# Optimization experiments

Measured on AMD Instinct MI355X. Metric: run time of the kernel, lower is better.

## Reference

```python
import jax, jax.numpy as jnp
import numpy as np
from jax import lax


def get_grid(h, w):
    # normalized [-1,1] grid, channel 0 = x, channel 1 = y, shape [1,h,w,2]
    gx, gy = jnp.meshgrid(jnp.linspace(-1.0, 1.0, w), jnp.linspace(-1.0, 1.0, h))
    return jnp.stack([gx, gy], axis=-1)[None].astype(jnp.float32)


def gaussian_kernel(k, sigma=1.0):
    c = jnp.arange(k, dtype=jnp.float32) - (k - 1) / 2.0
    g = jnp.exp(-(c ** 2) / (2.0 * sigma ** 2))
    k2 = jnp.outer(g, g)
    return k2 / k2.sum()


def resize_bilinear(x, H, W):
    # x: [B,C,h,w]; torch F.interpolate(mode='bilinear', align_corners=False)
    B, C, h, w = x.shape
    def coords(n_out, n_in):
        c = (jnp.arange(n_out, dtype=jnp.float32) + 0.5) * (n_in / n_out) - 0.5
        c = jnp.clip(c, 0.0, n_in - 1.0)
        lo = jnp.floor(c).astype(jnp.int32)
        hi = jnp.minimum(lo + 1, n_in - 1)
        return lo, hi, c - lo.astype(jnp.float32)
    y0, y1, wy = coords(H, h)
    x0, x1, wx = coords(W, w)
    r = x[:, :, y0, :] * (1.0 - wy)[None, None, :, None] + x[:, :, y1, :] * wy[None, None, :, None]
    return r[:, :, :, x0] * (1.0 - wx) + r[:, :, :, x1] * wx


def _forward(src_grid, kernel, src_grid_base, tgt_grid, niter):
    B = src_grid.shape[0]
    H, W = tgt_grid.shape[1], tgt_grid.shape[2]
    ks = kernel.shape[-1]
    HW = H * W
    # forward displacement, resampled to target resolution, in pixel units
    dsrc = (src_grid - src_grid_base).transpose(0, 3, 1, 2)        # [B,2,Hs,Ws]
    dsrc = resize_bilinear(dsrc, H, W)                              # [B,2,H,W]
    dx = dsrc[:, 0].reshape(B, HW) * (W / 2.0)
    dy = dsrc[:, 1].reshape(B, HW) * (H / 2.0)
    xg = (jnp.arange(HW) % W).astype(jnp.float32)
    yg = (jnp.arange(HW) // W).astype(jnp.float32)
    xi = jnp.round(xg[None] + dx).astype(jnp.int32)
    yi = jnp.round(yg[None] + dy).astype(jnp.int32)
    oob = (xi < 0) | (yi < 0) | (xi > W - 1) | (yi > H - 1)
    field = jnp.where(oob, -1, yi * W + xi) + 1   # index 0 = trash slot
    # sort + dedup: duplicates are redirected to the trash slot
    order = jnp.argsort(field, axis=1)            # stable
    sf = jnp.take_along_axis(field, order, axis=1)
    keep = jnp.concatenate([jnp.ones((B, 1), bool), sf[:, 1:] != sf[:, :-1]], axis=1)
    sf = sf * keep
    inv_order = jnp.argsort(order, axis=1)
    field = jnp.take_along_axis(sf, inv_order, axis=1)
    # scatter inverse displacement (unique indices except trash slot 0)
    z = jnp.zeros((B, 1), dtype=dx.dtype)
    dxp = jnp.concatenate([z, dx], axis=1)
    dyp = jnp.concatenate([z, dy], axis=1)
    fieldp = jnp.concatenate([jnp.zeros((B, 1), field.dtype), field], axis=1)
    bidx = jnp.arange(B)[:, None]
    inv_dx = jnp.zeros_like(dxp).at[bidx, fieldp].set(-dxp)[:, 1:].reshape(B, H, W)
    inv_dy = jnp.zeros_like(dyp).at[bidx, fieldp].set(-dyp)[:, 1:].reshape(B, H, W)
    mask = (jnp.zeros_like(dxp).at[bidx, fieldp].set(1.0)[:, 1:].reshape(B, H, W)) > 0.5
    # pad so hole-fill never reads outside
    p = niter + 1
    inv_dx = jnp.pad(inv_dx, ((0, 0), (p, p), (p, p)))
    inv_dy = jnp.pad(inv_dy, ((0, 0), (p, p), (p, p)))
    mask = jnp.pad(mask, ((0, 0), (p, p), (p, p)))
    pd = ks // 2
    k4 = kernel.reshape(1, 1, ks, ks)
    def conv(x):
        return lax.conv_general_dilated(x[:, None], k4, (1, 1), [(pd, pd), (pd, pd)])[:, 0]
    # hole-fill: dilate mask by 4-neighborhood, fill with gaussian-weighted avg
    for _ in range(niter):
        nb = (jnp.pad(mask, ((0, 0), (1, 0), (0, 0)))[:, :-1]
              | jnp.pad(mask, ((0, 0), (0, 1), (0, 0)))[:, 1:]
              | jnp.pad(mask, ((0, 0), (0, 0), (1, 0)))[:, :, :-1]
              | jnp.pad(mask, ((0, 0), (0, 0), (0, 1)))[:, :, 1:])
        new_mask = (~mask) & nb
        new_dx = conv(inv_dx)
        new_dy = conv(inv_dy)
        new_sum = conv(mask.astype(inv_dx.dtype))
        denom = jnp.where(new_mask, new_sum, 1.0)  # safe: new_sum>0 where new_mask
        inv_dx = jnp.where(new_mask, new_dx / denom, inv_dx)
        inv_dy = jnp.where(new_mask, new_dy / denom, inv_dy)
        mask = mask | new_mask
    # erode: drop pixels with any unmasked 4-neighbor (outside counts as masked)
    for _ in range(niter):
        full = (jnp.pad(mask, ((0, 0), (1, 0), (0, 0)), constant_values=True)[:, :-1]
                & jnp.pad(mask, ((0, 0), (0, 1), (0, 0)), constant_values=True)[:, 1:]
                & jnp.pad(mask, ((0, 0), (0, 0), (1, 0)), constant_values=True)[:, :, :-1]
                & jnp.pad(mask, ((0, 0), (0, 0), (0, 1)), constant_values=True)[:, :, 1:])
        mask = mask & full
    inv_dx = jnp.where(mask, inv_dx, 2.0 * W)
    inv_dy = jnp.where(mask, inv_dy, 2.0 * H)
    inv_dx = inv_dx[:, p:-p, p:-p]
    inv_dy = inv_dy[:, p:-p, p:-p]
    dtgt = jnp.stack([inv_dx * (2.0 / W), inv_dy * (2.0 / H)], axis=3)
    return tgt_grid + dtgt


def setup_inputs() -> dict:
    key = jax.random.key(0)
    B, Hs, Ws, H, W = 8, 256, 256, 512, 512
    base = get_grid(Hs, Ws)
    src_grid = base + 0.05 * jax.random.normal(key, (B, Hs, Ws, 2), jnp.float32)
    return {
        "src_grid": src_grid,
        "kernel": gaussian_kernel(3),
        "src_grid_base": base,
        "tgt_grid": get_grid(H, W),
        "niter": 5,
    }


def reference(src_grid, kernel, src_grid_base, tgt_grid, niter):
    return _forward(src_grid, kernel, src_grid_base, tgt_grid, niter)
```

## Files before the change

kernel.cpp:

```cpp
#include <hip/hip_runtime.h>
#include <hip/hip_fp16.h>

typedef unsigned long long u64;
typedef unsigned int u32;
typedef float float4a __attribute__((ext_vector_type(4), aligned(4)));

#define B_    8
#define HS_   256
#define WS_   256
#define H_    512
#define W_    512
#define HW_   (H_ * W_)
#define TO_Y  8
#define NTILE 64
#define WR    28
#define WCOLS 276
#define WSTR  277
#define NBAND 32
#define NBKT  64
#define INFW  0xFFFFFFFFu
#define CAPB  8192

__device__ __forceinline__ void bilin_disp(const float* __restrict__ src,
                                           const float* __restrict__ base,
                                           int b, int y, int x,
                                           float& dx, float& dy) {
#pragma clang fp contract(off)
    float cy = ((float)y + 0.5f) * 0.5f - 0.5f;
    cy = fminf(fmaxf(cy, 0.0f), 255.0f);
    int   y0 = (int)floorf(cy);
    int   y1 = min(y0 + 1, HS_ - 1);
    float wy = cy - (float)y0;

    float cx = ((float)x + 0.5f) * 0.5f - 0.5f;
    cx = fminf(fmaxf(cx, 0.0f), 255.0f);
    int   x0 = (int)floorf(cx);
    float wx = cx - (float)x0;

    float omy = 1.0f - wy;
    float wA, wB;
    int xs;
    if (x0 >= WS_ - 1) { xs = WS_ - 2; wA = 0.0f; wB = 1.0f; }
    else               { xs = x0;      wA = 1.0f - wx; wB = wx; }

    const float4a* S0 = (const float4a*)(src  + ((b * HS_ + y0) * WS_ + xs) * 2);
    const float4a* S1 = (const float4a*)(src  + ((b * HS_ + y1) * WS_ + xs) * 2);
    const float4a* B0 = (const float4a*)(base + (y0 * WS_ + xs) * 2);
    const float4a* B1 = (const float4a*)(base + (y1 * WS_ + xs) * 2);
    float4a s0 = *S0, s1 = *S1, b0 = *B0, b1 = *B1;

    float a00x = s0.x - b0.x, a00y = s0.y - b0.y;
    float a01x = s0.z - b0.z, a01y = s0.w - b0.w;
    float a10x = s1.x - b1.x, a10y = s1.y - b1.y;
    float a11x = s1.z - b1.z, a11y = s1.w - b1.w;

    float r0x = a00x * omy + a10x * wy;
    float r0y = a00y * omy + a10y * wy;
    float r1x = a01x * omy + a11x * wy;
    float r1y = a01y * omy + a11y * wy;
    dx = (r0x * wA + r1x * wB) * 256.0f;
    dy = (r0y * wA + r1y * wB) * 256.0f;
}

__device__ __forceinline__ u32 pack16(float x, float y) {
    __half hx = __float2half_rn(x), hy = __float2half_rn(y);
    return ((u32)__half_as_ushort(hy) << 16) | (u32)__half_as_ushort(hx);
}
__device__ __forceinline__ float2 unpack16(u32 p) {
    float2 f;
    f.x = __half2float(__ushort_as_half((unsigned short)(p & 0xFFFFu)));
    f.y = __half2float(__ushort_as_half((unsigned short)(p >> 16)));
    return f;
}

__device__ __forceinline__ u64 shfl_left(u64 v) {
    unsigned lo = __shfl_up((unsigned)v, 1);
    unsigned hi = __shfl_up((unsigned)(v >> 32), 1);
    u64 r = ((u64)hi << 32) | lo;
    return (threadIdx.x & 63) ? r : 0ull;
}
__device__ __forceinline__ u64 shfl_right(u64 v) {
    unsigned lo = __shfl_down((unsigned)v, 1);
    unsigned hi = __shfl_down((unsigned)(v >> 32), 1);
    u64 r = ((u64)hi << 32) | lo;
    return ((threadIdx.x & 63) == 63) ? 0ull : r;
}

__launch_bounds__(1024)
__global__ void pre_k(const float* __restrict__ src,
                      const float* __restrict__ base,
                      u32* __restrict__ pay,
                      u32* __restrict__ gcount,
                      u32* __restrict__ bucket) {
    __shared__ u32 cnt[NBKT];
    __shared__ u32 bbase[NBKT];

    int bid = blockIdx.x;
    int b   = bid & 7;
    int t   = bid >> 3;
    int j   = t * 1024 + threadIdx.x;
    int y   = j >> 9;
    int x   = j & (W_ - 1);

    if (threadIdx.x < NBKT) cnt[threadIdx.x] = 0;
    __syncthreads();

    float dx, dy;
    bilin_disp(src, base, b, y, x, dx, dy);
    pay[b * HW_ + j] = pack16(-dx, -dy);

    int xi = (int)rintf((float)x + dx);
    int yi = (int)rintf((float)y + dy);
    bool inb = (xi >= 0 && xi < W_ && yi >= 0 && yi < H_);
    int bk0 = 0, bk1 = -1;
    u32 r0 = 0, r1 = 0, e = 0;
    if (inb) {
        int band = yi >> 4;
        bk0 = band * 2 + (xi >> 8);
        r0 = atomicAdd(&cnt[bk0], 1u);
        if      (xi >= 246 && xi <= 255) bk1 = band * 2 + 1;
        else if (xi >= 256 && xi <= 265) bk1 = band * 2;
        if (bk1 >= 0) r1 = atomicAdd(&cnt[bk1], 1u);
        e = ((u32)(yi & 15) << 27) | ((u32)xi << 18) | (u32)j;
    }
    __syncthreads();
    if (threadIdx.x < NBKT) {
        u32 c = cnt[threadIdx.x];
        bbase[threadIdx.x] = c ? atomicAdd(&gcount[b * NBKT + threadIdx.x], c)
                               : 0u;
    }
    __syncthreads();
    if (inb) {
        u32 s0 = bbase[bk0] + r0;
        if (s0 < CAPB) bucket[(b * NBKT + bk0) * CAPB + s0] = e;
        if (bk1 >= 0) {
            u32 s1 = bbase[bk1] + r1;
            if (s1 < CAPB) bucket[(b * NBKT + bk1) * CAPB + s1] = e;
        }
    }
}

__launch_bounds__(512, 2)
__global__ void fused5_k(const u32* __restrict__ pay,
                         const u32* __restrict__ gcount,
                         const u32* __restrict__ bucket,
                         const float* __restrict__ kern,
                         const float* __restrict__ tgt,
                         float* __restrict__ out) {
    __shared__ u32 plane[WR * WSTR];

    int id   = blockIdx.x;
    int b    = id & 7;
    int rest = id >> 3;
    int tile = rest >> 1;
    int half = rest & 1;
    int X0   = half << 8;
    int Y0   = tile * TO_Y;
    int w0   = Y0 - 10;
    int wc0  = X0 - 10;
    int tid  = threadIdx.x;

    float kw[9];
#pragma unroll
    for (int q = 0; q < 9; q++) kw[q] = kern[q];

    for (int i = tid; i < WR * WSTR; i += 512) plane[i] = INFW;
    __syncthreads();

    {
        int qlo = max(0, w0 >> 4);
        int qhi = min(NBAND - 1, (w0 + WR - 1) >> 4);
        for (int q = qlo; q <= qhi; q++) {
            int bki = b * NBKT + q * 2 + half;
            u32 cntq = min(gcount[bki], (u32)CAPB);
            const u32* bk = bucket + bki * CAPB;
            int ybase = q * 16 - w0;
            for (u32 i = tid; i < cntq; i += 512) {
                u32 e  = bk[i];
                int wr = ybase + (int)((e >> 27) & 15u);
                if ((unsigned)wr < WR) {
                    int xc = (int)((e >> 18) & 511u) - wc0;
                    atomicMin(&plane[wr * WSTR + xc], e & 0x3FFFFu);
                }
            }
        }
    }
    __syncthreads();

    int wv   = tid >> 6;
    int lane = tid & 63;
    int col  = X0 + 32 * wv - 16 + lane;
    int cls  = col - wc0;
    bool inwin = ((unsigned)cls < WCOLS);
    bool colin = inwin && (col >= -6) && (col <= W_ + 5);

    u64 m = 0;
    if (colin) {
#pragma unroll 7
        for (int r = 0; r < WR; r++)
            m |= (u64)(plane[r * WSTR + cls] != INFW) << r;
    }
    __syncthreads();

    {
        const u32* pb = pay + b * HW_;
        for (int idx = tid; idx < WR * WCOLS; idx += 512) {
            int rr = idx / WCOLS;
            int cc = idx - rr * WCOLS;
            int off = rr * WSTR + cc;
            u32 k = plane[off];
            plane[off] = (k != INFW) ? pb[k] : 0u;
        }
    }
    __syncthreads();

    int rlo = max(0, -6 - w0);
    int rhi = min(WR - 1, (W_ + 5) - w0);
    u64 validm = colin ? ((((u64)1 << (rhi - rlo + 1)) - 1) << rlo) : 0ull;

    const u64 VROWS = (((u64)1 << (WR - 12)) - 1) << 6;
    bool vlane = (lane >= 6 && lane <= 57);

    for (int it = 0; it < 5; it++) {
        u64 mL = shfl_left(m), mR = shfl_right(m);
        u64 cand = ~m & ((m << 1) | (m >> 1) | mL | mR) & validm;
        u64 cv = vlane ? (cand & VROWS) : 0ull;
        while (cv) {
            int r = __builtin_ctzll(cv);
            cv &= cv - 1;
            float s = 0.0f, ax = 0.0f, ay = 0.0f;
#pragma unroll
            for (int dr = -1; dr <= 1; dr++) {
#pragma unroll
                for (int dc = -1; dc <= 1; dc++) {
                    if (dr == 0 && dc == 0) continue;
                    u64 nm = (dc < 0) ? mL : ((dc > 0) ? mR : m);
                    float wq = ((nm >> (r + dr)) & 1)
                                 ? kw[(dr + 1) * 3 + (dc + 1)] : 0.0f;
                    int cc = min(max(cls + dc, 0), WCOLS - 1);
                    float2 nv = unpack16(plane[(r + dr) * WSTR + cc]);
                    s += wq; ax += wq * nv.x; ay += wq * nv.y;
                }
            }
            float rs = __builtin_amdgcn_rcpf(s);
            plane[r * WSTR + cls] = pack16(ax * rs, ay * rs);
        }
        m |= cand;
        __syncthreads();
    }

    for (int it = 0; it < 5; it++) {
        u64 mL = shfl_left(m), mR = shfl_right(m);
        m &= (m << 1) & (m >> 1) & mL & mR;
    }

    if (lane >= 16 && lane < 48) {
#pragma unroll 4
        for (int r = 10; r < 10 + TO_Y; r++) {
            int row = w0 + r;
            bool on = (m >> r) & 1;
            float vx, vy;
            if (on) {
                float2 t = unpack16(plane[r * WSTR + cls]);
                vx = t.x * (1.0f / 256.0f);
                vy = t.y * (1.0f / 256.0f);
            } else {
                vx = 4.0f; vy = 4.0f;
            }
            int ti = (row * W_ + col) * 2;
            float2 tg = *(const float2*)(tgt + ti);
            float2 ov; ov.x = tg.x + vx; ov.y = tg.y + vy;
            ((float2*)out)[(size_t)b * HW_ + row * W_ + col] = ov;
        }
    }
}

extern "C" void kernel_launch(void* const* d_in, const int* in_sizes, int n_in,
                              void* d_out, int out_size, void* d_ws, size_t ws_size,
                              hipStream_t stream) {
    const float* src  = (const float*)d_in[0];
    const float* kern = (const float*)d_in[1];
    const float* base = (const float*)d_in[2];
    const float* tgt  = (const float*)d_in[3];
    float* out = (float*)d_out;

    char* ws = (char*)d_ws;
    u32* gcount = (u32*)ws;
    u32* pay    = (u32*)(ws + 4096);
    u32* bucket = (u32*)(ws + 4096 + (size_t)B_ * HW_ * 4);

    hipMemsetAsync(gcount, 0, B_ * NBKT * sizeof(u32), stream);

    pre_k<<<(B_ * HW_) / 1024, 1024, 0, stream>>>(src, base, pay, gcount, bucket);
    fused5_k<<<1024, 512, 0, stream>>>(pay, gcount, bucket, kern, tgt, out);
}
```

Before: 142.8 us.

## Replace bucketed scatter with dense 64-bit atomicMin field carrying payload

```diff
diff --git a/kernel.cpp b/kernel.cpp
--- a/kernel.cpp
+++ b/kernel.cpp
@@ -16,10 +16,7 @@
 #define WR    28
 #define WCOLS 276
 #define WSTR  277
-#define NBAND 32
-#define NBKT  64
 #define INFW  0xFFFFFFFFu
-#define CAPB  8192
 
 __device__ __forceinline__ void bilin_disp(const float* __restrict__ src,
                                            const float* __restrict__ base,
@@ -89,12 +86,7 @@
 __launch_bounds__(1024)
 __global__ void pre_k(const float* __restrict__ src,
                       const float* __restrict__ base,
-                      u32* __restrict__ pay,
-                      u32* __restrict__ gcount,
-                      u32* __restrict__ bucket) {
-    __shared__ u32 cnt[NBKT];
-    __shared__ u32 bbase[NBKT];
-
+                      u64* __restrict__ field) {
     int bid = blockIdx.x;
     int b   = bid & 7;
     int t   = bid >> 3;
@@ -102,48 +94,19 @@
     int y   = j >> 9;
     int x   = j & (W_ - 1);
 
-    if (threadIdx.x < NBKT) cnt[threadIdx.x] = 0;
-    __syncthreads();
-
     float dx, dy;
     bilin_disp(src, base, b, y, x, dx, dy);
-    pay[b * HW_ + j] = pack16(-dx, -dy);
+    u32 pk = pack16(-dx, -dy);
 
     int xi = (int)rintf((float)x + dx);
     int yi = (int)rintf((float)y + dy);
-    bool inb = (xi >= 0 && xi < W_ && yi >= 0 && yi < H_);
-    int bk0 = 0, bk1 = -1;
-    u32 r0 = 0, r1 = 0, e = 0;
-    if (inb) {
-        int band = yi >> 4;
-        bk0 = band * 2 + (xi >> 8);
-        r0 = atomicAdd(&cnt[bk0], 1u);
-        if      (xi >= 246 && xi <= 255) bk1 = band * 2 + 1;
-        else if (xi >= 256 && xi <= 265) bk1 = band * 2;
-        if (bk1 >= 0) r1 = atomicAdd(&cnt[bk1], 1u);
-        e = ((u32)(yi & 15) << 27) | ((u32)xi << 18) | (u32)j;
-    }
-    __syncthreads();
-    if (threadIdx.x < NBKT) {
-        u32 c = cnt[threadIdx.x];
-        bbase[threadIdx.x] = c ? atomicAdd(&gcount[b * NBKT + threadIdx.x], c)
-                               : 0u;
-    }
-    __syncthreads();
-    if (inb) {
-        u32 s0 = bbase[bk0] + r0;
-        if (s0 < CAPB) bucket[(b * NBKT + bk0) * CAPB + s0] = e;
-        if (bk1 >= 0) {
-            u32 s1 = bbase[bk1] + r1;
-            if (s1 < CAPB) bucket[(b * NBKT + bk1) * CAPB + s1] = e;
-        }
-    }
+    if (xi >= 0 && xi < W_ && yi >= 0 && yi < H_)
+        atomicMin(&field[(size_t)b * HW_ + (yi << 9) + xi],
+                  ((u64)j << 32) | (u64)pk);
 }
 
 __launch_bounds__(512, 2)
-__global__ void fused5_k(const u32* __restrict__ pay,
-                         const u32* __restrict__ gcount,
-                         const u32* __restrict__ bucket,
+__global__ void fused5_k(const u64* __restrict__ field,
                          const float* __restrict__ kern,
                          const float* __restrict__ tgt,
                          float* __restrict__ out) {
@@ -164,25 +127,19 @@
 #pragma unroll
     for (int q = 0; q < 9; q++) kw[q] = kern[q];
 
-    for (int i = tid; i < WR * WSTR; i += 512) plane[i] = INFW;
-    __syncthreads();
-
     {
-        int qlo = max(0, w0 >> 4);
-        int qhi = min(NBAND - 1, (w0 + WR - 1) >> 4);
-        for (int q = qlo; q <= qhi; q++) {
-            int bki = b * NBKT + q * 2 + half;
-            u32 cntq = min(gcount[bki], (u32)CAPB);
-            const u32* bk = bucket + bki * CAPB;
-            int ybase = q * 16 - w0;
-            for (u32 i = tid; i < cntq; i += 512) {
-                u32 e  = bk[i];
-                int wr = ybase + (int)((e >> 27) & 15u);
-                if ((unsigned)wr < WR) {
-                    int xc = (int)((e >> 18) & 511u) - wc0;
-                    atomicMin(&plane[wr * WSTR + xc], e & 0x3FFFFu);
-                }
+        const u64* fb = field + (size_t)b * HW_;
+        for (int idx = tid; idx < WR * WCOLS; idx += 512) {
+            int rr  = idx / WCOLS;
+            int cc  = idx - rr * WCOLS;
+            int row = w0 + rr;
+            int col = wc0 + cc;
+            u32 v = INFW;
+            if ((unsigned)row < (unsigned)H_ && (unsigned)col < (unsigned)W_) {
+                u64 f = fb[(row << 9) + col];
+                if ((u32)(f >> 32) != INFW) v = (u32)f;
             }
+            plane[rr * WSTR + cc] = v;
         }
     }
     __syncthreads();
@@ -202,15 +159,8 @@
     }
     __syncthreads();
 
-    {
-        const u32* pb = pay + b * HW_;
-        for (int idx = tid; idx < WR * WCOLS; idx += 512) {
-            int rr = idx / WCOLS;
-            int cc = idx - rr * WCOLS;
-            int off = rr * WSTR + cc;
-            u32 k = plane[off];
-            plane[off] = (k != INFW) ? pb[k] : 0u;
-        }
+    for (int i = tid; i < WR * WSTR; i += 512) {
+        if (plane[i] == INFW) plane[i] = 0u;
     }
     __syncthreads();
 
@@ -284,13 +234,10 @@
     const float* tgt  = (const float*)d_in[3];
     float* out = (float*)d_out;
 
-    char* ws = (char*)d_ws;
-    u32* gcount = (u32*)ws;
-    u32* pay    = (u32*)(ws + 4096);
-    u32* bucket = (u32*)(ws + 4096 + (size_t)B_ * HW_ * 4);
-
-    hipMemsetAsync(gcount, 0, B_ * NBKT * sizeof(u32), stream);
-
-    pre_k<<<(B_ * HW_) / 1024, 1024, 0, stream>>>(src, base, pay, gcount, bucket);
-    fused5_k<<<1024, 512, 0, stream>>>(pay, gcount, bucket, kern, tgt, out);
-}
+    u64* field = (u64*)d_ws;
+
+    hipMemsetAsync(field, 0xFF, (size_t)B_ * HW_ * sizeof(u64), stream);
+
+    pre_k<<<(B_ * HW_) / 1024, 1024, 0, stream>>>(src, base, field);
+    fused5_k<<<1024, 512, 0, stream>>>(field, kern, tgt, out);
+}
```

Result: slower. 199.5 us (+39.6%).
